# Performance work log

Hardware: AMD Instinct MI355X
Metric: run time of the kernel (lower is better)

Reference implementation:

```python
import jax, jax.numpy as jnp
import numpy as np

T, H, F, E, K = 4096, 2048, 1408, 8, 2  # tokens, hidden, intermediate, experts, top_k


def setup_inputs() -> dict:
    key = jax.random.key(0)
    k1, k2, k3, k4 = jax.random.split(key, 4)
    return {
        "hidden_states": jax.random.normal(k1, (T, H), dtype=jnp.float32),
        "router_logits": jax.random.normal(k2, (T, E), dtype=jnp.float32),
        # w1: (E, 2, H, F) where dim 1 = [gate_proj, up_proj]
        "w1": jax.random.normal(k3, (E, 2, H, F), dtype=jnp.float32) * 0.02,
        # w2: (E, F, H) down projection
        "w2": jax.random.normal(k4, (E, F, H), dtype=jnp.float32) * 0.02,
        "top_k": K,
    }


def reference(hidden_states, router_logits, w1, w2, top_k):
    # Router: softmax over all experts, then select top_k.
    # renormalize_topk_logits=False -> combine weights are the raw softmax probs.
    probs = jax.nn.softmax(router_logits, axis=-1)            # (T, E)
    topk_w, topk_ids = jax.lax.top_k(probs, top_k)            # (T, K) each

    num_experts = w1.shape[0]
    out = jnp.zeros_like(hidden_states)                       # (T, H)
    # Fixed small loop over experts (structurally distinct weight slices);
    # each expert's FFN is a dense GEMM over all tokens, masked by the
    # per-token combine coefficient (0 for tokens not routed to this expert).
    for e in range(num_experts):
        coef = jnp.sum(jnp.where(topk_ids == e, topk_w, 0.0), axis=-1)  # (T,)
        gate = hidden_states @ w1[e, 0]                       # (T, F)
        up = hidden_states @ w1[e, 1]                         # (T, F)
        h = jax.nn.silu(gate) * up                            # SwiGLU
        out = out + coef[:, None] * (h @ w2[e])               # (T, H)
    return out
```

## Files before the change

kernel.cpp:

```cpp
#include <hip/hip_runtime.h>
#include <stdint.h>

#define T_TOK 4096
#define HID   2048
#define FF    1408
#define NE    8

typedef __attribute__((ext_vector_type(8))) short short8;
typedef __attribute__((ext_vector_type(4))) float f32x4;

__device__ inline unsigned short f2bf(float f) {
  uint32_t u = __builtin_bit_cast(uint32_t, f);
  u += 0x7fffu + ((u >> 16) & 1u);
  return (unsigned short)(u >> 16);
}

__device__ inline uint32_t cvt_pk(float a, float b) {
  uint32_t r;
  asm("v_cvt_pk_bf16_f32 %0, %1, %2" : "=v"(r) : "v"(a), "v"(b));
  return r;
}

__device__ inline void gload16(const void* g, void* l) {
  __builtin_amdgcn_global_load_lds(
      (const __attribute__((address_space(1))) unsigned int*)g,
      (__attribute__((address_space(3))) unsigned int*)l, 16, 0, 0);
}

__device__ inline void vm0_barrier() {
  asm volatile("s_waitcnt vmcnt(0)" ::: "memory");
  __builtin_amdgcn_s_barrier();
  asm volatile("" ::: "memory");
}

__global__ __launch_bounds__(256) void route_kernel(const float* __restrict__ logits,
                                                    int2* __restrict__ eids,
                                                    float2* __restrict__ ecfs) {
  int t = blockIdx.x * 256 + threadIdx.x;
  const float4* lp = (const float4*)(logits + (size_t)t * NE);
  float4 a = lp[0], b = lp[1];
  float l[8] = {a.x, a.y, a.z, a.w, b.x, b.y, b.z, b.w};
  float mx = l[0];
#pragma unroll
  for (int i = 1; i < 8; ++i) mx = fmaxf(mx, l[i]);
  float s = 0.f, p[8];
#pragma unroll
  for (int i = 0; i < 8; ++i) { p[i] = __expf(l[i] - mx); s += p[i]; }
  float inv = 1.f / s;
  int e0 = 0;
#pragma unroll
  for (int i = 1; i < 8; ++i) if (l[i] > l[e0]) e0 = i;
  int e1 = (e0 == 0) ? 1 : 0;
#pragma unroll
  for (int i = 0; i < 8; ++i) if (i != e0 && l[i] > l[e1]) e1 = i;
  eids[t] = make_int2(e0, e1);
  ecfs[t] = make_float2(p[e0] * inv, p[e1] * inv);
}

__global__ __launch_bounds__(256) void compact_kernel(const int2* __restrict__ eids,
                                                      const float2* __restrict__ ecfs,
                                                      int* __restrict__ tok,
                                                      float* __restrict__ coef,
                                                      int* __restrict__ rowptr) {
  int e = blockIdx.x, tid = threadIdx.x;
  __shared__ int hist[8];
  __shared__ int wsum[4];
  __shared__ int runv;
  if (tid < 8) hist[tid] = 0;
  __syncthreads();
  for (int t = tid; t < T_TOK; t += 256) {
    int2 ei = eids[t];
    atomicAdd(&hist[ei.x], 1);
    atomicAdd(&hist[ei.y], 1);
  }
  __syncthreads();
  int off = 0;
  for (int j = 0; j < e; ++j) off += hist[j];
  if (tid == 0) {
    runv = 0;
    if (e == 0) rowptr[0] = 0;
    rowptr[e + 1] = off + hist[e];
  }
  __syncthreads();
  int wave = tid >> 6, lane = tid & 63;
  for (int c = 0; c < T_TOK; c += 256) {
    int t = c + tid;
    int2 ei = eids[t];
    float2 cf = ecfs[t];
    bool fl = false; float cv = 0.f;
    if (ei.x == e)      { fl = true; cv = cf.x; }
    else if (ei.y == e) { fl = true; cv = cf.y; }
    unsigned long long m = __ballot(fl);
    if (lane == 0) wsum[wave] = __popcll(m);
    __syncthreads();
    int woff = runv;
    for (int wv = 0; wv < wave; ++wv) woff += wsum[wv];
    int pos = off + woff + __popcll(m & ((1ull << lane) - 1ull));
    if (fl) { tok[pos] = t; coef[pos] = cv; }
    __syncthreads();
    if (tid == 0) runv += wsum[0] + wsum[1] + wsum[2] + wsum[3];
    __syncthreads();
  }
}

__global__ __launch_bounds__(256) void cvtx_kernel(const float* __restrict__ x,
                                                   unsigned short* __restrict__ xb) {
  int i = blockIdx.x * 256 + threadIdx.x;
  float4 v = ((const float4*)x)[i];
  uint2 o;
  o.x = cvt_pk(v.x, v.y);
  o.y = cvt_pk(v.z, v.w);
  ((uint2*)xb)[i] = o;
}

__global__ __launch_bounds__(256) void wcvt_kernel(const float* __restrict__ in,
                                                   unsigned short* __restrict__ out,
                                                   int R, int C) {
  __shared__ unsigned short t[64][72];
  const float* ip = in + ((size_t)blockIdx.z * R + blockIdx.y * 64) * C + blockIdx.x * 64;
  int tid = threadIdx.x;
  int r = tid >> 2, cg = (tid & 3) * 16;
  const float* rp = ip + (size_t)r * C + cg;
#pragma unroll
  for (int j = 0; j < 4; ++j) {
    float4 v = *(const float4*)(rp + j * 4);
    int c = cg + j * 4;
    t[c + 0][r] = f2bf(v.x);
    t[c + 1][r] = f2bf(v.y);
    t[c + 2][r] = f2bf(v.z);
    t[c + 3][r] = f2bf(v.w);
  }
  __syncthreads();
  int cr = tid >> 2, kg = (tid & 3) * 16;
  unsigned short* op = out + ((size_t)blockIdx.z * C + blockIdx.x * 64 + cr) * R +
                       blockIdx.y * 64 + kg;
  *(short8*)op = *(const short8*)&t[cr][kg];
  *(short8*)(op + 8) = *(const short8*)&t[cr][kg + 8];
}

__global__ __launch_bounds__(256) void gemm1_kernel(const unsigned short* __restrict__ Xb,
                                                    const unsigned short* __restrict__ w1t,
                                                    const int* __restrict__ tok,
                                                    const int* __restrict__ rowptr,
                                                    unsigned short* __restrict__ hbuf) {
  int f = blockIdx.x + 22 * blockIdx.y;
  int g = (f & 7) * 88 + (f >> 3);
  int ftile = g >> 5, mtile = g & 31;
  int e = blockIdx.z;
  int base = rowptr[e], cnt = rowptr[e + 1] - base;
  if (mtile * 128 >= cnt) return;
  __shared__ char As[2][8192];
  __shared__ char Bs[2][8192];
  int tid = threadIdx.x, lane = tid & 63, wave = tid >> 6;

  int rA = wave * 32 + (lane >> 2);
  int cd = (lane & 3) ^ ((rA >> 1) & 3);
  int sA0 = min(mtile * 128 + rA, cnt - 1);
  int sA1 = min(mtile * 128 + rA + 16, cnt - 1);
  const unsigned short* gA0 = Xb + (size_t)tok[base + sA0] * HID + cd * 8;
  const unsigned short* gA1 = Xb + (size_t)tok[base + sA1] * HID + cd * 8;
  int r1 = rA + 16;
  int p0 = (rA >> 4) & 1, f0 = (rA & 15) + 16 * (rA >> 5);
  int p1 = (r1 >> 4) & 1, f1 = (r1 & 15) + 16 * (r1 >> 5);
  const unsigned short* gB0 = w1t + ((size_t)(e * 2 + p0) * FF + ftile * 64 + f0) * HID + cd * 8;
  const unsigned short* gB1 = w1t + ((size_t)(e * 2 + p1) * FF + ftile * 64 + f1) * HID + cd * 8;
  int lb = wave * 2048;

#define STAGE1(buf, k0) do {                       \
    gload16(gA0 + (k0), As[buf] + lb);             \
    gload16(gA1 + (k0), As[buf] + lb + 1024);      \
    gload16(gB0 + (k0), Bs[buf] + lb);             \
    gload16(gB1 + (k0), Bs[buf] + lb + 1024);      \
  } while (0)

  int wm = wave >> 1, wn = wave & 1, kc = lane >> 4;
  int aoff[4], boff[4];
#pragma unroll
  for (int mi = 0; mi < 4; ++mi) {
    int row = wm * 64 + mi * 16 + (lane & 15);
    aoff[mi] = row * 64 + ((kc ^ ((row >> 1) & 3)) << 4);
  }
#pragma unroll
  for (int ni = 0; ni < 4; ++ni) {
    int n = wn * 64 + ni * 16 + (lane & 15);
    boff[ni] = n * 64 + ((kc ^ ((n >> 1) & 3)) << 4);
  }

  const f32x4 vz = {0.f, 0.f, 0.f, 0.f};
  f32x4 acc[4][4];
#pragma unroll
  for (int mi = 0; mi < 4; ++mi)
#pragma unroll
    for (int ni = 0; ni < 4; ++ni) acc[mi][ni] = vz;

  STAGE1(0, 0);
  vm0_barrier();
#pragma unroll 2
  for (int it = 0; it < HID / 32; ++it) {
    int cur = it & 1;
    int k0 = it * 32;
    if (it + 1 < HID / 32) STAGE1(cur ^ 1, k0 + 32);
    short8 af[4], bb[4];
#pragma unroll
    for (int mi = 0; mi < 4; ++mi) af[mi] = *(const short8*)(As[cur] + aoff[mi]);
#pragma unroll
    for (int ni = 0; ni < 4; ++ni) bb[ni] = *(const short8*)(Bs[cur] + boff[ni]);
#pragma unroll
    for (int mi = 0; mi < 4; ++mi)
#pragma unroll
      for (int ni = 0; ni < 4; ++ni)
        acc[mi][ni] = __builtin_amdgcn_mfma_f32_16x16x32_bf16(af[mi], bb[ni], acc[mi][ni], 0, 0, 0);
    vm0_barrier();
  }
#undef STAGE1

  int fb = ftile * 64 + wn * 32 + (lane & 15);
#pragma unroll
  for (int mi = 0; mi < 4; ++mi) {
#pragma unroll
    for (int i = 0; i < 4; ++i) {
      int ml = wm * 64 + mi * 16 + (lane >> 4) * 4 + i;
      int slot = mtile * 128 + ml;
      if (slot < cnt) {
        size_t hrow = (size_t)(base + slot) * FF + fb;
        float g0 = acc[mi][0][i], u0 = acc[mi][1][i];
        float g1 = acc[mi][2][i], u1 = acc[mi][3][i];
        hbuf[hrow]      = f2bf(g0 / (1.f + __expf(-g0)) * u0);
        hbuf[hrow + 16] = f2bf(g1 / (1.f + __expf(-g1)) * u1);
      }
    }
  }
}

__global__ __launch_bounds__(256) void gemm2_kernel(const unsigned short* __restrict__ hbuf,
                                                    const unsigned short* __restrict__ w2t,
                                                    const int* __restrict__ tok,
                                                    const float* __restrict__ coef,
                                                    const int* __restrict__ rowptr,
                                                    float* __restrict__ out) {
  int f = blockIdx.x + 16 * blockIdx.y;
  int g = (f & 7) * 64 + (f >> 3);
  int ntile = g >> 5, mtile = g & 31;
  int e = blockIdx.z;
  int base = rowptr[e], cnt = rowptr[e + 1] - base;
  if (mtile * 128 >= cnt) return;
  __shared__ char As[2][8192];
  __shared__ char Bs[2][8192];
  __shared__ int tokL[128];
  __shared__ float cofL[128];
  int tid = threadIdx.x, lane = tid & 63, wave = tid >> 6;
  if (tid < 128) {
    int slot = min(mtile * 128 + tid, cnt - 1);
    tokL[tid] = tok[base + slot];
    cofL[tid] = coef[base + slot];
  }
  __syncthreads();

  int rA = wave * 32 + (lane >> 2);
  int cd = (lane & 3) ^ ((rA >> 1) & 3);
  int sA0 = min(mtile * 128 + rA, cnt - 1);
  int sA1 = min(mtile * 128 + rA + 16, cnt - 1);
  const unsigned short* gA0 = hbuf + (size_t)(base + sA0) * FF + cd * 8;
  const unsigned short* gA1 = hbuf + (size_t)(base + sA1) * FF + cd * 8;
  const unsigned short* gB0 = w2t + ((size_t)e * HID + ntile * 128 + rA) * FF + cd * 8;
  const unsigned short* gB1 = gB0 + (size_t)16 * FF;
  int lb = wave * 2048;

#define STAGE2(buf, k0) do {                       \
    gload16(gA0 + (k0), As[buf] + lb);             \
    gload16(gA1 + (k0), As[buf] + lb + 1024);      \
    gload16(gB0 + (k0), Bs[buf] + lb);             \
    gload16(gB1 + (k0), Bs[buf] + lb + 1024);      \
  } while (0)

  int wm = wave >> 1, wn = wave & 1, kc = lane >> 4;
  int aoff[4], boff[4];
#pragma unroll
  for (int mi = 0; mi < 4; ++mi) {
    int row = wm * 64 + mi * 16 + (lane & 15);
    aoff[mi] = row * 64 + ((kc ^ ((row >> 1) & 3)) << 4);
  }
#pragma unroll
  for (int ni = 0; ni < 4; ++ni) {
    int n = wn * 64 + ni * 16 + (lane & 15);
    boff[ni] = n * 64 + ((kc ^ ((n >> 1) & 3)) << 4);
  }

  const f32x4 vz = {0.f, 0.f, 0.f, 0.f};
  f32x4 acc[4][4];
#pragma unroll
  for (int mi = 0; mi < 4; ++mi)
#pragma unroll
    for (int ni = 0; ni < 4; ++ni) acc[mi][ni] = vz;

  STAGE2(0, 0);
  vm0_barrier();
#pragma unroll 2
  for (int it = 0; it < FF / 32; ++it) {
    int cur = it & 1;
    int k0 = it * 32;
    if (it + 1 < FF / 32) STAGE2(cur ^ 1, k0 + 32);
    short8 af[4], bb[4];
#pragma unroll
    for (int mi = 0; mi < 4; ++mi) af[mi] = *(const short8*)(As[cur] + aoff[mi]);
#pragma unroll
    for (int ni = 0; ni < 4; ++ni) bb[ni] = *(const short8*)(Bs[cur] + boff[ni]);
#pragma unroll
    for (int mi = 0; mi < 4; ++mi)
#pragma unroll
      for (int ni = 0; ni < 4; ++ni)
        acc[mi][ni] = __builtin_amdgcn_mfma_f32_16x16x32_bf16(af[mi], bb[ni], acc[mi][ni], 0, 0, 0);
    vm0_barrier();
  }
#undef STAGE2

#pragma unroll
  for (int mi = 0; mi < 4; ++mi) {
#pragma unroll
    for (int i = 0; i < 4; ++i) {
      int ml = wm * 64 + mi * 16 + (lane >> 4) * 4 + i;
      int slot = mtile * 128 + ml;
      if (slot < cnt) {
        float cf = cofL[ml];
        float* op = out + (size_t)tokL[ml] * HID + ntile * 128 + wn * 64 + (lane & 15);
#pragma unroll
        for (int ni = 0; ni < 4; ++ni)
          unsafeAtomicAdd(op + ni * 16, cf * acc[mi][ni][i]);
      }
    }
  }
}

extern "C" void kernel_launch(void* const* d_in, const int* in_sizes, int n_in,
                              void* d_out, int out_size, void* d_ws, size_t ws_size,
                              hipStream_t stream) {
  const float* X  = (const float*)d_in[0];
  const float* RL = (const float*)d_in[1];
  const float* W1 = (const float*)d_in[2];
  const float* W2 = (const float*)d_in[3];
  float* out = (float*)d_out;

  const size_t OFF_EIDS = 4096;
  const size_t OFF_ECFS = 36864;
  const size_t OFF_TOK  = 69632;
  const size_t OFF_COEF = 102400;
  const size_t OFF_XB   = 135168;
  const size_t OFF_H    = 16912384;
  const size_t OFF_W1T  = 39981056;
  const size_t OFF_W2T  = 132255744;
  const size_t TOTAL2   = 178393088;
  if (ws_size < TOTAL2 || n_in < 4) return;

  char* w = (char*)d_ws;
  int*    rowptr = (int*)w;
  int2*   eids   = (int2*)(w + OFF_EIDS);
  float2* ecfs   = (float2*)(w + OFF_ECFS);
  int*    tok    = (int*)(w + OFF_TOK);
  float*  coef   = (float*)(w + OFF_COEF);
  unsigned short* Xb   = (unsigned short*)(w + OFF_XB);
  unsigned short* hbuf = (unsigned short*)(w + OFF_H);
  unsigned short* w1t  = (unsigned short*)(w + OFF_W1T);
  unsigned short* w2t  = (unsigned short*)(w + OFF_W2T);

  hipMemsetAsync(d_out, 0, (size_t)T_TOK * HID * sizeof(float), stream);
  route_kernel<<<T_TOK / 256, 256, 0, stream>>>(RL, eids, ecfs);
  compact_kernel<<<NE, 256, 0, stream>>>(eids, ecfs, tok, coef, rowptr);
  cvtx_kernel<<<(T_TOK * HID / 4) / 256, 256, 0, stream>>>(X, Xb);
  wcvt_kernel<<<dim3(FF / 64, HID / 64, NE * 2), 256, 0, stream>>>(W1, w1t, HID, FF);
  wcvt_kernel<<<dim3(HID / 64, FF / 64, NE), 256, 0, stream>>>(W2, w2t, FF, HID);
  gemm1_kernel<<<dim3(FF / 64, T_TOK / 128, NE), 256, 0, stream>>>(Xb, w1t, tok, rowptr, hbuf);
  gemm2_kernel<<<dim3(HID / 128, T_TOK / 128, NE), 256, 0, stream>>>(hbuf, w2t, tok, coef, rowptr, out);
}
```

Baseline: 400.4 us.

## Triple-buffer LDS staging in both MoE GEMMs with partial vmcnt waits

Both grouped GEMM kernels move from double-buffered LDS to a three-stage ring, issuing global-to-LDS loads two k-steps ahead. Each iteration now waits with vmcnt(4) instead of vmcnt(0), so the next tile's loads can stay in flight across the barrier. The MFMA block is also wrapped in s_setprio to favour math issue. The cost is that LDS per block grows from 32KB to 48KB, which may lower occupancy, and the loop is no longer unrolled by 2.

```diff
diff --git a/kernel.cpp b/kernel.cpp
--- a/kernel.cpp
+++ b/kernel.cpp
@@ -5,6 +5,9 @@
 #define HID   2048
 #define FF    1408
 #define NE    8
+#define BUF   16384
+#define NT1   (HID / 32)
+#define NT2   (FF / 32)
 
 typedef __attribute__((ext_vector_type(8))) short short8;
 typedef __attribute__((ext_vector_type(4))) float f32x4;
@@ -27,7 +30,12 @@
       (__attribute__((address_space(3))) unsigned int*)l, 16, 0, 0);
 }
 
-__device__ inline void vm0_barrier() {
+__device__ inline void wait4_barrier() {
+  asm volatile("s_waitcnt vmcnt(4)" ::: "memory");
+  __builtin_amdgcn_s_barrier();
+  asm volatile("" ::: "memory");
+}
+__device__ inline void wait0_barrier() {
   asm volatile("s_waitcnt vmcnt(0)" ::: "memory");
   __builtin_amdgcn_s_barrier();
   asm volatile("" ::: "memory");
@@ -149,8 +157,7 @@
   int e = blockIdx.z;
   int base = rowptr[e], cnt = rowptr[e + 1] - base;
   if (mtile * 128 >= cnt) return;
-  __shared__ char As[2][8192];
-  __shared__ char Bs[2][8192];
+  __shared__ char smem[3 * BUF];
   int tid = threadIdx.x, lane = tid & 63, wave = tid >> 6;
 
   int rA = wave * 32 + (lane >> 2);
@@ -164,13 +171,13 @@
   int p1 = (r1 >> 4) & 1, f1 = (r1 & 15) + 16 * (r1 >> 5);
   const unsigned short* gB0 = w1t + ((size_t)(e * 2 + p0) * FF + ftile * 64 + f0) * HID + cd * 8;
   const unsigned short* gB1 = w1t + ((size_t)(e * 2 + p1) * FF + ftile * 64 + f1) * HID + cd * 8;
-  int lb = wave * 2048;
-
-#define STAGE1(buf, k0) do {                       \
-    gload16(gA0 + (k0), As[buf] + lb);             \
-    gload16(gA1 + (k0), As[buf] + lb + 1024);      \
-    gload16(gB0 + (k0), Bs[buf] + lb);             \
-    gload16(gB1 + (k0), Bs[buf] + lb + 1024);      \
+  int lb = wave * 2048 + lane * 16;
+
+#define STG1(bp, k0) do {                          \
+    gload16(gA0 + (k0), (bp) + lb);                \
+    gload16(gA1 + (k0), (bp) + lb + 1024);         \
+    gload16(gB0 + (k0), (bp) + 8192 + lb);         \
+    gload16(gB1 + (k0), (bp) + 8192 + lb + 1024);  \
   } while (0)
 
   int wm = wave >> 1, wn = wave & 1, kc = lane >> 4;
@@ -183,7 +190,7 @@
 #pragma unroll
   for (int ni = 0; ni < 4; ++ni) {
     int n = wn * 64 + ni * 16 + (lane & 15);
-    boff[ni] = n * 64 + ((kc ^ ((n >> 1) & 3)) << 4);
+    boff[ni] = 8192 + n * 64 + ((kc ^ ((n >> 1) & 3)) << 4);
   }
 
   const f32x4 vz = {0.f, 0.f, 0.f, 0.f};
@@ -193,26 +200,32 @@
 #pragma unroll
     for (int ni = 0; ni < 4; ++ni) acc[mi][ni] = vz;
 
-  STAGE1(0, 0);
-  vm0_barrier();
-#pragma unroll 2
-  for (int it = 0; it < HID / 32; ++it) {
-    int cur = it & 1;
-    int k0 = it * 32;
-    if (it + 1 < HID / 32) STAGE1(cur ^ 1, k0 + 32);
+  STG1(smem, 0);
+  STG1(smem + BUF, 32);
+  wait4_barrier();
+
+  char* cur = smem;
+  char* nxt = smem + 2 * BUF;
+  for (int t = 0; t < NT1; ++t) {
+    bool pf = (t + 2) < NT1;
+    if (pf) STG1(nxt, (t + 2) * 32);
     short8 af[4], bb[4];
 #pragma unroll
-    for (int mi = 0; mi < 4; ++mi) af[mi] = *(const short8*)(As[cur] + aoff[mi]);
-#pragma unroll
-    for (int ni = 0; ni < 4; ++ni) bb[ni] = *(const short8*)(Bs[cur] + boff[ni]);
+    for (int mi = 0; mi < 4; ++mi) af[mi] = *(const short8*)(cur + aoff[mi]);
+#pragma unroll
+    for (int ni = 0; ni < 4; ++ni) bb[ni] = *(const short8*)(cur + boff[ni]);
+    __builtin_amdgcn_s_setprio(1);
 #pragma unroll
     for (int mi = 0; mi < 4; ++mi)
 #pragma unroll
       for (int ni = 0; ni < 4; ++ni)
         acc[mi][ni] = __builtin_amdgcn_mfma_f32_16x16x32_bf16(af[mi], bb[ni], acc[mi][ni], 0, 0, 0);
-    vm0_barrier();
-  }
-#undef STAGE1
+    __builtin_amdgcn_s_setprio(0);
+    if (pf) wait4_barrier(); else wait0_barrier();
+    cur = (cur == smem + 2 * BUF) ? smem : cur + BUF;
+    nxt = (nxt == smem + 2 * BUF) ? smem : nxt + BUF;
+  }
+#undef STG1
 
   int fb = ftile * 64 + wn * 32 + (lane & 15);
 #pragma unroll
@@ -244,8 +257,7 @@
   int e = blockIdx.z;
   int base = rowptr[e], cnt = rowptr[e + 1] - base;
   if (mtile * 128 >= cnt) return;
-  __shared__ char As[2][8192];
-  __shared__ char Bs[2][8192];
+  __shared__ char smem[3 * BUF];
   __shared__ int tokL[128];
   __shared__ float cofL[128];
   int tid = threadIdx.x, lane = tid & 63, wave = tid >> 6;
@@ -264,13 +276,13 @@
   const unsigned short* gA1 = hbuf + (size_t)(base + sA1) * FF + cd * 8;
   const unsigned short* gB0 = w2t + ((size_t)e * HID + ntile * 128 + rA) * FF + cd * 8;
   const unsigned short* gB1 = gB0 + (size_t)16 * FF;
-  int lb = wave * 2048;
-
-#define STAGE2(buf, k0) do {                       \
-    gload16(gA0 + (k0), As[buf] + lb);             \
-    gload16(gA1 + (k0), As[buf] + lb + 1024);      \
-    gload16(gB0 + (k0), Bs[buf] + lb);             \
-    gload16(gB1 + (k0), Bs[buf] + lb + 1024);      \
+  int lb = wave * 2048 + lane * 16;
+
+#define STG2(bp, k0) do {                          \
+    gload16(gA0 + (k0), (bp) + lb);                \
+    gload16(gA1 + (k0), (bp) + lb + 1024);         \
+    gload16(gB0 + (k0), (bp) + 8192 + lb);         \
+    gload16(gB1 + (k0), (bp) + 8192 + lb + 1024);  \
   } while (0)
 
   int wm = wave >> 1, wn = wave & 1, kc = lane >> 4;
@@ -283,7 +295,7 @@
 #pragma unroll
   for (int ni = 0; ni < 4; ++ni) {
     int n = wn * 64 + ni * 16 + (lane & 15);
-    boff[ni] = n * 64 + ((kc ^ ((n >> 1) & 3)) << 4);
+    boff[ni] = 8192 + n * 64 + ((kc ^ ((n >> 1) & 3)) << 4);
   }
 
   const f32x4 vz = {0.f, 0.f, 0.f, 0.f};
@@ -293,26 +305,32 @@
 #pragma unroll
     for (int ni = 0; ni < 4; ++ni) acc[mi][ni] = vz;
 
-  STAGE2(0, 0);
-  vm0_barrier();
-#pragma unroll 2
-  for (int it = 0; it < FF / 32; ++it) {
-    int cur = it & 1;
-    int k0 = it * 32;
-    if (it + 1 < FF / 32) STAGE2(cur ^ 1, k0 + 32);
+  STG2(smem, 0);
+  STG2(smem + BUF, 32);
+  wait4_barrier();
+
+  char* cur = smem;
+  char* nxt = smem + 2 * BUF;
+  for (int t = 0; t < NT2; ++t) {
+    bool pf = (t + 2) < NT2;
+    if (pf) STG2(nxt, (t + 2) * 32);
     short8 af[4], bb[4];
 #pragma unroll
-    for (int mi = 0; mi < 4; ++mi) af[mi] = *(const short8*)(As[cur] + aoff[mi]);
-#pragma unroll
-    for (int ni = 0; ni < 4; ++ni) bb[ni] = *(const short8*)(Bs[cur] + boff[ni]);
+    for (int mi = 0; mi < 4; ++mi) af[mi] = *(const short8*)(cur + aoff[mi]);
+#pragma unroll
+    for (int ni = 0; ni < 4; ++ni) bb[ni] = *(const short8*)(cur + boff[ni]);
+    __builtin_amdgcn_s_setprio(1);
 #pragma unroll
     for (int mi = 0; mi < 4; ++mi)
 #pragma unroll
       for (int ni = 0; ni < 4; ++ni)
         acc[mi][ni] = __builtin_amdgcn_mfma_f32_16x16x32_bf16(af[mi], bb[ni], acc[mi][ni], 0, 0, 0);
-    vm0_barrier();
-  }
-#undef STAGE2
+    __builtin_amdgcn_s_setprio(0);
+    if (pf) wait4_barrier(); else wait0_barrier();
+    cur = (cur == smem + 2 * BUF) ? smem : cur + BUF;
+    nxt = (nxt == smem + 2 * BUF) ? smem : nxt + BUF;
+  }
+#undef STG2
 
 #pragma unroll
   for (int mi = 0; mi < 4; ++mi) {
```

Result: faster. 368.6 us (-7.9%).

## Enlarge expert GEMM tiles to 256-row blocks with 8 waves and BK=64

Applied to the files above, without the earlier changes.

Both grouped GEMMs move from 128x64/128x128 tiles with 256 threads and a K-step of 32 to 256x128/256x256 tiles with 512 threads, a K-step of 64 and a 128 KB double-buffered LDS region using an XOR swizzle. The MFMA issue is split into four phases per K-step, each with a barrier and s_setprio raised around the MFMAs, to interleave LDS reads with matrix math across waves. The aim is more data reuse per byte loaded and fewer loop iterations. The cost is far fewer blocks, so with about a thousand tokens per expert the CUs may be poorly balanced, and only one block fits per CU because of the LDS size.

```diff
diff --git a/kernel.cpp b/kernel.cpp
--- a/kernel.cpp
+++ b/kernel.cpp
@@ -5,6 +5,10 @@
 #define HID   2048
 #define FF    1408
 #define NE    8
+#define SLOT  65536
+#define BREG  32768
+#define NT1   (HID / 64)
+#define NT2   (FF / 64)
 
 typedef __attribute__((ext_vector_type(8))) short short8;
 typedef __attribute__((ext_vector_type(4))) float f32x4;
@@ -138,191 +142,201 @@
   *(short8*)(op + 8) = *(const short8*)&t[cr][kg + 8];
 }
 
-__global__ __launch_bounds__(256) void gemm1_kernel(const unsigned short* __restrict__ Xb,
-                                                    const unsigned short* __restrict__ w1t,
-                                                    const int* __restrict__ tok,
-                                                    const int* __restrict__ rowptr,
-                                                    unsigned short* __restrict__ hbuf) {
-  int f = blockIdx.x + 22 * blockIdx.y;
-  int g = (f & 7) * 88 + (f >> 3);
-  int ftile = g >> 5, mtile = g & 31;
-  int e = blockIdx.z;
+#define PHASE(S, q) do {                                                      \
+    short8 aA = *(const short8*)((S) + aoff[2*(q)]);                          \
+    short8 aB = *(const short8*)((S) + (aoff[2*(q)] ^ 64));                   \
+    short8 aC = *(const short8*)((S) + aoff[2*(q)+1]);                        \
+    short8 aD = *(const short8*)((S) + (aoff[2*(q)+1] ^ 64));                 \
+    __builtin_amdgcn_s_barrier();                                             \
+    __builtin_amdgcn_s_setprio(1);                                            \
+    _Pragma("unroll")                                                         \
+    for (int ni = 0; ni < 4; ++ni) {                                          \
+      acc[2*(q)][ni]   = __builtin_amdgcn_mfma_f32_16x16x32_bf16(aA, bb[ni][0], acc[2*(q)][ni], 0, 0, 0);   \
+      acc[2*(q)][ni]   = __builtin_amdgcn_mfma_f32_16x16x32_bf16(aB, bb[ni][1], acc[2*(q)][ni], 0, 0, 0);   \
+      acc[2*(q)+1][ni] = __builtin_amdgcn_mfma_f32_16x16x32_bf16(aC, bb[ni][0], acc[2*(q)+1][ni], 0, 0, 0); \
+      acc[2*(q)+1][ni] = __builtin_amdgcn_mfma_f32_16x16x32_bf16(aD, bb[ni][1], acc[2*(q)+1][ni], 0, 0, 0); \
+    }                                                                         \
+    __builtin_amdgcn_s_setprio(0);                                            \
+  } while (0)
+
+__global__ __launch_bounds__(512, 2) void gemm1_kernel(const unsigned short* __restrict__ Xb,
+                                                       const unsigned short* __restrict__ w1t,
+                                                       const int* __restrict__ tok,
+                                                       const int* __restrict__ rowptr,
+                                                       unsigned short* __restrict__ hbuf) {
+  int mtile = blockIdx.x, ntile = blockIdx.y, e = blockIdx.z;
   int base = rowptr[e], cnt = rowptr[e + 1] - base;
-  if (mtile * 128 >= cnt) return;
-  __shared__ char As[2][8192];
-  __shared__ char Bs[2][8192];
+  if (mtile * 256 >= cnt) return;
+  __shared__ char smem[2 * SLOT];
   int tid = threadIdx.x, lane = tid & 63, wave = tid >> 6;
-
-  int rA = wave * 32 + (lane >> 2);
-  int cd = (lane & 3) ^ ((rA >> 1) & 3);
-  int sA0 = min(mtile * 128 + rA, cnt - 1);
-  int sA1 = min(mtile * 128 + rA + 16, cnt - 1);
-  const unsigned short* gA0 = Xb + (size_t)tok[base + sA0] * HID + cd * 8;
-  const unsigned short* gA1 = Xb + (size_t)tok[base + sA1] * HID + cd * 8;
-  int r1 = rA + 16;
-  int p0 = (rA >> 4) & 1, f0 = (rA & 15) + 16 * (rA >> 5);
-  int p1 = (r1 >> 4) & 1, f1 = (r1 & 15) + 16 * (r1 >> 5);
-  const unsigned short* gB0 = w1t + ((size_t)(e * 2 + p0) * FF + ftile * 64 + f0) * HID + cd * 8;
-  const unsigned short* gB1 = w1t + ((size_t)(e * 2 + p1) * FF + ftile * 64 + f1) * HID + cd * 8;
-  int lb = wave * 2048;
-
-#define STAGE1(buf, k0) do {                       \
-    gload16(gA0 + (k0), As[buf] + lb);             \
-    gload16(gA1 + (k0), As[buf] + lb + 1024);      \
-    gload16(gB0 + (k0), Bs[buf] + lb);             \
-    gload16(gB1 + (k0), Bs[buf] + lb + 1024);      \
+  int wm = wave >> 2, wn = wave & 3;
+
+  int p = tid & 7, rr = tid >> 3;
+  const unsigned short* gA[4];
+  const unsigned short* gB[4];
+#pragma unroll
+  for (int c = 0; c < 4; ++c) {
+    int row = 64 * c + rr;
+    int ch = p ^ (row & 7);
+    int slot = min(mtile * 256 + row, cnt - 1);
+    gA[c] = Xb + (size_t)tok[base + slot] * HID + ch * 8;
+    int proj = (row >> 4) & 1;
+    int fg = ntile * 128 + (row & 15) + 16 * (row >> 5);
+    gB[c] = w1t + ((size_t)(e * 2 + proj) * FF + fg) * HID + ch * 8;
+  }
+  int ldst = tid * 16;
+
+#define STG1(sb, k0) do {                                         \
+    _Pragma("unroll") for (int c = 0; c < 4; ++c)                 \
+      gload16(gA[c] + (k0), smem + (sb) + c * 8192 + ldst);       \
+    _Pragma("unroll") for (int c = 0; c < 4; ++c)                 \
+      gload16(gB[c] + (k0), smem + (sb) + BREG + c * 8192 + ldst);\
   } while (0)
 
-  int wm = wave >> 1, wn = wave & 1, kc = lane >> 4;
-  int aoff[4], boff[4];
-#pragma unroll
-  for (int mi = 0; mi < 4; ++mi) {
-    int row = wm * 64 + mi * 16 + (lane & 15);
-    aoff[mi] = row * 64 + ((kc ^ ((row >> 1) & 3)) << 4);
+  int g = lane >> 4, j = lane & 15;
+  int aoff[8], boff[4];
+#pragma unroll
+  for (int mi = 0; mi < 8; ++mi) {
+    int row = wm * 128 + mi * 16 + j;
+    aoff[mi] = row * 128 + ((g ^ (row & 7)) << 4);
   }
 #pragma unroll
   for (int ni = 0; ni < 4; ++ni) {
-    int n = wn * 64 + ni * 16 + (lane & 15);
-    boff[ni] = n * 64 + ((kc ^ ((n >> 1) & 3)) << 4);
+    int row = wn * 64 + ni * 16 + j;
+    boff[ni] = BREG + row * 128 + ((g ^ (row & 7)) << 4);
   }
 
   const f32x4 vz = {0.f, 0.f, 0.f, 0.f};
-  f32x4 acc[4][4];
-#pragma unroll
-  for (int mi = 0; mi < 4; ++mi)
+  f32x4 acc[8][4];
+#pragma unroll
+  for (int mi = 0; mi < 8; ++mi)
 #pragma unroll
     for (int ni = 0; ni < 4; ++ni) acc[mi][ni] = vz;
 
-  STAGE1(0, 0);
+  STG1(0, 0);
   vm0_barrier();
-#pragma unroll 2
-  for (int it = 0; it < HID / 32; ++it) {
-    int cur = it & 1;
-    int k0 = it * 32;
-    if (it + 1 < HID / 32) STAGE1(cur ^ 1, k0 + 32);
-    short8 af[4], bb[4];
-#pragma unroll
-    for (int mi = 0; mi < 4; ++mi) af[mi] = *(const short8*)(As[cur] + aoff[mi]);
-#pragma unroll
-    for (int ni = 0; ni < 4; ++ni) bb[ni] = *(const short8*)(Bs[cur] + boff[ni]);
-#pragma unroll
-    for (int mi = 0; mi < 4; ++mi)
-#pragma unroll
-      for (int ni = 0; ni < 4; ++ni)
-        acc[mi][ni] = __builtin_amdgcn_mfma_f32_16x16x32_bf16(af[mi], bb[ni], acc[mi][ni], 0, 0, 0);
+
+  for (int t = 0; t < NT1; ++t) {
+    char* S = smem + (t & 1) * SLOT;
+    if (t + 1 < NT1) STG1(((t + 1) & 1) * SLOT, (t + 1) * 64);
+    short8 bb[4][2];
+#pragma unroll
+    for (int ni = 0; ni < 4; ++ni) {
+      bb[ni][0] = *(const short8*)(S + boff[ni]);
+      bb[ni][1] = *(const short8*)(S + (boff[ni] ^ 64));
+    }
+    PHASE(S, 0);
+    PHASE(S, 1);
+    PHASE(S, 2);
+    PHASE(S, 3);
     vm0_barrier();
   }
-#undef STAGE1
-
-  int fb = ftile * 64 + wn * 32 + (lane & 15);
-#pragma unroll
-  for (int mi = 0; mi < 4; ++mi) {
+#undef STG1
+
+  int fb0 = ntile * 128 + j;
+#pragma unroll
+  for (int mi = 0; mi < 8; ++mi) {
 #pragma unroll
     for (int i = 0; i < 4; ++i) {
-      int ml = wm * 64 + mi * 16 + (lane >> 4) * 4 + i;
-      int slot = mtile * 128 + ml;
+      int r = wm * 128 + mi * 16 + g * 4 + i;
+      int slot = mtile * 256 + r;
       if (slot < cnt) {
-        size_t hrow = (size_t)(base + slot) * FF + fb;
-        float g0 = acc[mi][0][i], u0 = acc[mi][1][i];
-        float g1 = acc[mi][2][i], u1 = acc[mi][3][i];
-        hbuf[hrow]      = f2bf(g0 / (1.f + __expf(-g0)) * u0);
-        hbuf[hrow + 16] = f2bf(g1 / (1.f + __expf(-g1)) * u1);
+        size_t hrow = (size_t)(base + slot) * FF + fb0;
+#pragma unroll
+        for (int pr = 0; pr < 2; ++pr) {
+          float gg = acc[mi][2 * pr][i], uu = acc[mi][2 * pr + 1][i];
+          float hv = gg / (1.f + __expf(-gg)) * uu;
+          hbuf[hrow + 16 * (2 * wn + pr)] = f2bf(hv);
+        }
       }
     }
   }
 }
 
-__global__ __launch_bounds__(256) void gemm2_kernel(const unsigned short* __restrict__ hbuf,
-                                                    const unsigned short* __restrict__ w2t,
-                                                    const int* __restrict__ tok,
-                                                    const float* __restrict__ coef,
-                                                    const int* __restrict__ rowptr,
-                                                    float* __restrict__ out) {
-  int f = blockIdx.x + 16 * blockIdx.y;
-  int g = (f & 7) * 64 + (f >> 3);
-  int ntile = g >> 5, mtile = g & 31;
-  int e = blockIdx.z;
+__global__ __launch_bounds__(512, 2) void gemm2_kernel(const unsigned short* __restrict__ hbuf,
+                                                       const unsigned short* __restrict__ w2t,
+                                                       const int* __restrict__ tok,
+                                                       const float* __restrict__ coef,
+                                                       const int* __restrict__ rowptr,
+                                                       float* __restrict__ out) {
+  int mtile = blockIdx.x, ntile = blockIdx.y, e = blockIdx.z;
   int base = rowptr[e], cnt = rowptr[e + 1] - base;
-  if (mtile * 128 >= cnt) return;
-  __shared__ char As[2][8192];
-  __shared__ char Bs[2][8192];
-  __shared__ int tokL[128];
-  __shared__ float cofL[128];
+  if (mtile * 256 >= cnt) return;
+  __shared__ char smem[2 * SLOT];
   int tid = threadIdx.x, lane = tid & 63, wave = tid >> 6;
-  if (tid < 128) {
-    int slot = min(mtile * 128 + tid, cnt - 1);
-    tokL[tid] = tok[base + slot];
-    cofL[tid] = coef[base + slot];
-  }
-  __syncthreads();
-
-  int rA = wave * 32 + (lane >> 2);
-  int cd = (lane & 3) ^ ((rA >> 1) & 3);
-  int sA0 = min(mtile * 128 + rA, cnt - 1);
-  int sA1 = min(mtile * 128 + rA + 16, cnt - 1);
-  const unsigned short* gA0 = hbuf + (size_t)(base + sA0) * FF + cd * 8;
-  const unsigned short* gA1 = hbuf + (size_t)(base + sA1) * FF + cd * 8;
-  const unsigned short* gB0 = w2t + ((size_t)e * HID + ntile * 128 + rA) * FF + cd * 8;
-  const unsigned short* gB1 = gB0 + (size_t)16 * FF;
-  int lb = wave * 2048;
-
-#define STAGE2(buf, k0) do {                       \
-    gload16(gA0 + (k0), As[buf] + lb);             \
-    gload16(gA1 + (k0), As[buf] + lb + 1024);      \
-    gload16(gB0 + (k0), Bs[buf] + lb);             \
-    gload16(gB1 + (k0), Bs[buf] + lb + 1024);      \
+  int wm = wave >> 2, wn = wave & 3;
+
+  int p = tid & 7, rr = tid >> 3;
+  const unsigned short* gA[4];
+  const unsigned short* gB[4];
+#pragma unroll
+  for (int c = 0; c < 4; ++c) {
+    int row = 64 * c + rr;
+    int ch = p ^ (row & 7);
+    int slot = min(mtile * 256 + row, cnt - 1);
+    gA[c] = hbuf + (size_t)(base + slot) * FF + ch * 8;
+    gB[c] = w2t + ((size_t)e * HID + ntile * 256 + row) * FF + ch * 8;
+  }
+  int ldst = tid * 16;
+
+#define STG2(sb, k0) do {                                         \
+    _Pragma("unroll") for (int c = 0; c < 4; ++c)                 \
+      gload16(gA[c] + (k0), smem + (sb) + c * 8192 + ldst);       \
+    _Pragma("unroll") for (int c = 0; c < 4; ++c)                 \
+      gload16(gB[c] + (k0), smem + (sb) + BREG + c * 8192 + ldst);\
   } while (0)
 
-  int wm = wave >> 1, wn = wave & 1, kc = lane >> 4;
-  int aoff[4], boff[4];
-#pragma unroll
-  for (int mi = 0; mi < 4; ++mi) {
-    int row = wm * 64 + mi * 16 + (lane & 15);
-    aoff[mi] = row * 64 + ((kc ^ ((row >> 1) & 3)) << 4);
+  int g = lane >> 4, j = lane & 15;
+  int aoff[8], boff[4];
+#pragma unroll
+  for (int mi = 0; mi < 8; ++mi) {
+    int row = wm * 128 + mi * 16 + j;
+    aoff[mi] = row * 128 + ((g ^ (row & 7)) << 4);
   }
 #pragma unroll
   for (int ni = 0; ni < 4; ++ni) {
-    int n = wn * 64 + ni * 16 + (lane & 15);
-    boff[ni] = n * 64 + ((kc ^ ((n >> 1) & 3)) << 4);
+    int row = wn * 64 + ni * 16 + j;
+    boff[ni] = BREG + row * 128 + ((g ^ (row & 7)) << 4);
   }
 
   const f32x4 vz = {0.f, 0.f, 0.f, 0.f};
-  f32x4 acc[4][4];
-#pragma unroll
-  for (int mi = 0; mi < 4; ++mi)
+  f32x4 acc[8][4];
+#pragma unroll
+  for (int mi = 0; mi < 8; ++mi)
 #pragma unroll
     for (int ni = 0; ni < 4; ++ni) acc[mi][ni] = vz;
 
-  STAGE2(0, 0);
+  STG2(0, 0);
   vm0_barrier();
-#pragma unroll 2
-  for (int it = 0; it < FF / 32; ++it) {
-    int cur = it & 1;
-    int k0 = it * 32;
-    if (it + 1 < FF / 32) STAGE2(cur ^ 1, k0 + 32);
-    short8 af[4], bb[4];
-#pragma unroll
-    for (int mi = 0; mi < 4; ++mi) af[mi] = *(const short8*)(As[cur] + aoff[mi]);
-#pragma unroll
-    for (int ni = 0; ni < 4; ++ni) bb[ni] = *(const short8*)(Bs[cur] + boff[ni]);
-#pragma unroll
-    for (int mi = 0; mi < 4; ++mi)
-#pragma unroll
-      for (int ni = 0; ni < 4; ++ni)
-        acc[mi][ni] = __builtin_amdgcn_mfma_f32_16x16x32_bf16(af[mi], bb[ni], acc[mi][ni], 0, 0, 0);
+
+  for (int t = 0; t < NT2; ++t) {
+    char* S = smem + (t & 1) * SLOT;
+    if (t + 1 < NT2) STG2(((t + 1) & 1) * SLOT, (t + 1) * 64);
+    short8 bb[4][2];
+#pragma unroll
+    for (int ni = 0; ni < 4; ++ni) {
+      bb[ni][0] = *(const short8*)(S + boff[ni]);
+      bb[ni][1] = *(const short8*)(S + (boff[ni] ^ 64));
+    }
+    PHASE(S, 0);
+    PHASE(S, 1);
+    PHASE(S, 2);
+    PHASE(S, 3);
     vm0_barrier();
   }
-#undef STAGE2
-
-#pragma unroll
-  for (int mi = 0; mi < 4; ++mi) {
+#undef STG2
+
+  int nb = ntile * 256 + wn * 64 + j;
+#pragma unroll
+  for (int mi = 0; mi < 8; ++mi) {
 #pragma unroll
     for (int i = 0; i < 4; ++i) {
-      int ml = wm * 64 + mi * 16 + (lane >> 4) * 4 + i;
-      int slot = mtile * 128 + ml;
+      int r = wm * 128 + mi * 16 + g * 4 + i;
+      int slot = mtile * 256 + r;
       if (slot < cnt) {
-        float cf = cofL[ml];
-        float* op = out + (size_t)tokL[ml] * HID + ntile * 128 + wn * 64 + (lane & 15);
+        int tk = tok[base + slot];
+        float cf = coef[base + slot];
+        float* op = out + (size_t)tk * HID + nb;
 #pragma unroll
         for (int ni = 0; ni < 4; ++ni)
           unsafeAtomicAdd(op + ni * 16, cf * acc[mi][ni][i]);
@@ -368,6 +382,6 @@
   cvtx_kernel<<<(T_TOK * HID / 4) / 256, 256, 0, stream>>>(X, Xb);
   wcvt_kernel<<<dim3(FF / 64, HID / 64, NE * 2), 256, 0, stream>>>(W1, w1t, HID, FF);
   wcvt_kernel<<<dim3(HID / 64, FF / 64, NE), 256, 0, stream>>>(W2, w2t, FF, HID);
-  gemm1_kernel<<<dim3(FF / 64, T_TOK / 128, NE), 256, 0, stream>>>(Xb, w1t, tok, rowptr, hbuf);
-  gemm2_kernel<<<dim3(HID / 128, T_TOK / 128, NE), 256, 0, stream>>>(hbuf, w2t, tok, coef, rowptr, out);
-}
+  gemm1_kernel<<<dim3(32, FF / 128, NE), 512, 0, stream>>>(Xb, w1t, tok, rowptr, hbuf);
+  gemm2_kernel<<<dim3(32, HID / 256, NE), 512, 0, stream>>>(hbuf, w2t, tok, coef, rowptr, out);
+}
```

After: 1.164 ms. 2.91x slower.
